# Optimization experiments

Measured on AMD Instinct MI355X. Metric: run time of the kernel, lower is better.

## Reference

```python
import jax, jax.numpy as jnp
import numpy as np

D_MODEL = 192
D_INNER = 384   # expand=2
D_STATE = 16
D_CONV = 4
DT_RANK = 12    # ceil(192/16)
DEPTH = 4
STRIDE = 4
N_PATCH = 400   # 1600 // 4
NCLS = 1000
BATCH = 32
EPS = 1e-5


def setup_inputs() -> dict:
    key = jax.random.key(0)
    ks = iter(jax.random.split(key, 64))
    nrm = lambda shp, s=0.02: jax.random.normal(next(ks), shp, jnp.float32) * s
    inp = {}
    inp["imgs"] = jax.random.normal(next(ks), (BATCH, 1, 40, 40), jnp.float32)
    # StrideEmbed: conv1d(kernel=stride=4) == per-patch linear on [B,400,4]
    inp["patch_w"] = nrm((STRIDE, D_MODEL))
    inp["patch_b"] = jnp.zeros((D_MODEL,), jnp.float32)
    inp["cls_token"] = nrm((1, 1, D_MODEL))
    inp["pos_embed"] = nrm((1, N_PATCH + 1, D_MODEL))
    # per-block Mamba params, stacked on a leading depth axis
    inp["norm_ws"] = jnp.ones((DEPTH, D_MODEL), jnp.float32)
    inp["in_proj_ws"] = nrm((DEPTH, D_MODEL, 2 * D_INNER))
    inp["conv_ws"] = nrm((DEPTH, D_INNER, D_CONV), 0.2)
    inp["conv_bs"] = jnp.zeros((DEPTH, D_INNER), jnp.float32)
    inp["x_proj_ws"] = nrm((DEPTH, D_INNER, DT_RANK + 2 * D_STATE))
    inp["dt_proj_ws"] = nrm((DEPTH, DT_RANK, D_INNER), 0.1)
    # dt bias ~ inverse-softplus of small positive dt
    inp["dt_proj_bs"] = jnp.log(jnp.expm1(jnp.full((DEPTH, D_INNER), 0.01, jnp.float32)))
    inp["A_logs"] = jnp.log(jnp.broadcast_to(
        jnp.arange(1, D_STATE + 1, dtype=jnp.float32), (DEPTH, D_INNER, D_STATE)))
    inp["Ds"] = jnp.ones((DEPTH, D_INNER), jnp.float32)
    inp["out_proj_ws"] = nrm((DEPTH, D_INNER, D_MODEL))
    inp["norm_f_w"] = jnp.ones((D_MODEL,), jnp.float32)
    inp["head_w"] = nrm((D_MODEL, NCLS))
    inp["head_b"] = jnp.zeros((NCLS,), jnp.float32)
    return inp


def rmsnorm(x, w):
    return x * jax.lax.rsqrt(jnp.mean(x * x, axis=-1, keepdims=True) + EPS) * w


def mamba_mixer(x, in_w, conv_w, conv_b, xp_w, dt_w, dt_b, A_log, Dp, out_w):
    # x: [B, L, D_MODEL]
    B, L, _ = x.shape
    xz = x @ in_w                         # [B, L, 2*d_inner]
    u, z = jnp.split(xz, 2, axis=-1)
    # causal depthwise conv1d (kernel 4), truncated to L, then SiLU
    upad = jnp.pad(u, ((0, 0), (D_CONV - 1, 0), (0, 0)))
    uc = sum(upad[:, k:k + L, :] * conv_w[:, k] for k in range(D_CONV)) + conv_b
    uc = jax.nn.silu(uc)
    # input-dependent dt, B, C
    dbl = uc @ xp_w                       # [B, L, dt_rank + 2*d_state]
    dt = dbl[..., :DT_RANK]
    Bm = dbl[..., DT_RANK:DT_RANK + D_STATE]
    Cm = dbl[..., DT_RANK + D_STATE:]
    delta = jax.nn.softplus(dt @ dt_w + dt_b)           # [B, L, d_inner]
    A = -jnp.exp(A_log)                                  # [d_inner, d_state]
    dA = jnp.exp(delta[..., None] * A)                   # [B, L, d_inner, d_state]
    dBu = (delta * uc)[..., None] * Bm[:, :, None, :]    # [B, L, d_inner, d_state]

    def step(h, t):
        da, dbu, c = t
        h = da * h + dbu                                 # [B, d_inner, d_state]
        y = jnp.einsum('bds,bs->bd', h, c)
        return h, y

    h0 = jnp.zeros((B, D_INNER, D_STATE), x.dtype)
    _, ys = jax.lax.scan(step, h0, (jnp.moveaxis(dA, 1, 0),
                                    jnp.moveaxis(dBu, 1, 0),
                                    jnp.moveaxis(Cm, 1, 0)))
    y = jnp.moveaxis(ys, 0, 1) + uc * Dp                 # [B, L, d_inner]
    return (y * jax.nn.silu(z)) @ out_w


def reference(imgs, patch_w, patch_b, cls_token, pos_embed, norm_ws, in_proj_ws,
              conv_ws, conv_bs, x_proj_ws, dt_proj_ws, dt_proj_bs, A_logs, Ds,
              out_proj_ws, norm_f_w, head_w, head_b):
    B = imgs.shape[0]
    seq = imgs.reshape(B, N_PATCH, STRIDE)               # [B, 400, 4] (in_chans=1)
    x = seq @ patch_w + patch_b + pos_embed[:, :-1, :]   # patch embed + pos (cls pos is last)
    cls = cls_token + pos_embed[:, -1:, :]
    x = jnp.concatenate([x, jnp.broadcast_to(cls, (B, 1, D_MODEL))], axis=1)  # cls appended at end
    residual = None
    for i in range(DEPTH):
        residual = x if residual is None else x + residual  # fused add-norm, prenorm
        h = rmsnorm(residual, norm_ws[i])
        x = mamba_mixer(h, in_proj_ws[i], conv_ws[i], conv_bs[i], x_proj_ws[i],
                        dt_proj_ws[i], dt_proj_bs[i], A_logs[i], Ds[i], out_proj_ws[i])
    x = rmsnorm(x + residual, norm_f_w)                   # final fused add-norm, prenorm=False
    return x[:, -1, :] @ head_w + head_b                  # head on cls (last) token
```

## Files before the change

### kernel.cpp

```cpp
#include <hip/hip_runtime.h>
#include <hip/hip_bf16.h>
#include <hip/hip_fp16.h>

using bf16 = __hip_bfloat16;
typedef short short8 __attribute__((ext_vector_type(8)));
typedef float floatx4 __attribute__((ext_vector_type(4)));

#define LSEQ 401
#define NTOK 12832
#define NTOKP 12928
#define DM 192
#define DI 384
#define NB 32
#define NCH 13
#define CHT 32

#define O_IMGS   0
#define O_PW     51200
#define O_PB     51968
#define O_CLS    52160
#define O_POS    52352
#define O_NORMW  129344
#define O_INW    130112
#define O_CONVW  719936
#define O_CONVB  726080
#define O_XPW    727616
#define O_DTW    795200
#define O_DTB    813632
#define O_ALOG   815168
#define O_DS     839744
#define O_OUTW   841280
#define O_NORMF  1136192
#define O_HEADW  1136384
#define O_HEADB  1328384
#define WTOT     1329408

#define BO_INWT  0
#define BO_XPWT  589824
#define BO_OUTWT 688128
#define BFTOT_F  491520

__constant__ int g_sz[18] = {51200, 768, 192, 192, 76992, 768, 589824, 6144, 1536,
                             67584, 18432, 1536, 24576, 1536, 294912, 192, 192000, 1000};
__constant__ int g_off[18] = {O_IMGS, O_PW, O_PB, O_CLS, O_POS, O_NORMW, O_INW, O_CONVW,
                              O_CONVB, O_XPW, O_DTW, O_DTB, O_ALOG, O_DS, O_OUTW,
                              O_NORMF, O_HEADW, O_HEADB};

struct SrcPtrs { const void* p[18]; };

static __device__ __forceinline__ int probe_flag(const unsigned short* probe) {
    unsigned short u0 = probe[0];
    if (u0 == 0x3F80u) return 0;
    if (u0 == 0x3C00u) return 2;
    return 1;
}
static __device__ __forceinline__ float load_src(int flag, const void* p, long i) {
    if (flag == 0) return __bfloat162float(((const bf16*)p)[i]);
    if (flag == 2) return __half2float(((const __half*)p)[i]);
    return ((const float*)p)[i];
}
static __device__ __forceinline__ unsigned short f2b(float f) {
    bf16 h = __float2bfloat16(f);
    return *reinterpret_cast<unsigned short*>(&h);
}
static __device__ __forceinline__ float b2f_us(unsigned short us) {
    unsigned int ui = (unsigned int)us << 16;
    return __uint_as_float(ui);
}

__global__ void convert_kernel(SrcPtrs sp, const unsigned short* __restrict__ probe,
                               float* __restrict__ dst) {
    int flag = probe_flag(probe);
    int which = blockIdx.y;
    int n = g_sz[which];
    const void* src = sp.p[which];
    float* d = dst + g_off[which];
    for (int i = blockIdx.x * blockDim.x + threadIdx.x; i < n; i += gridDim.x * blockDim.x)
        d[i] = load_src(flag, src, i);
}

__global__ void prep_wt_kernel(SrcPtrs sp, const unsigned short* __restrict__ probe,
                               unsigned short* __restrict__ bfw) {
    int flag = probe_flag(probe);
    int which = blockIdx.y, layer = blockIdx.z;
    int i = blockIdx.x * 256 + threadIdx.x;
    if (which == 0) {
        if (i >= 768 * 192) return;
        int n = i / 192, k = i % 192;
        float v = load_src(flag, sp.p[6], (long)layer * 147456 + (long)k * 768 + n);
        bfw[BO_INWT + (long)layer * 147456 + i] = f2b(v);
    } else if (which == 1) {
        if (i >= 64 * 384) return;
        int n = i / 384, k = i % 384;
        float v = (n < 44) ? load_src(flag, sp.p[9], (long)layer * 16896 + (long)k * 44 + n) : 0.f;
        bfw[BO_XPWT + (long)layer * 24576 + i] = f2b(v);
    } else {
        if (i >= 192 * 384) return;
        int n = i / 384, k = i % 384;
        float v = load_src(flag, sp.p[14], (long)layer * 73728 + (long)k * 192 + n);
        bfw[BO_OUTWT + (long)layer * 73728 + i] = f2b(v);
    }
}

__global__ __launch_bounds__(192) void embed_kernel(const float* __restrict__ W, float* __restrict__ x) {
    const float* imgs = W + O_IMGS;
    const float* pw   = W + O_PW;
    int tok = blockIdx.x;
    int b = tok / LSEQ, t = tok % LSEQ;
    int c = threadIdx.x;
    float v;
    if (t < 400) {
        float s0 = imgs[b * 1600 + t * 4 + 0];
        float s1 = imgs[b * 1600 + t * 4 + 1];
        float s2 = imgs[b * 1600 + t * 4 + 2];
        float s3 = imgs[b * 1600 + t * 4 + 3];
        v = s0 * pw[0 * DM + c] + s1 * pw[1 * DM + c] +
            s2 * pw[2 * DM + c] + s3 * pw[3 * DM + c] +
            W[O_PB + c] + W[O_POS + t * DM + c];
    } else {
        v = W[O_CLS + c] + W[O_POS + 400 * DM + c];
    }
    x[(long)tok * DM + c] = v;
}

__global__ __launch_bounds__(256) void resnorm_kernel(
    const float* __restrict__ x, float* __restrict__ res, unsigned short* __restrict__ hbf,
    const float* __restrict__ w, int first) {
    int wv = threadIdx.x >> 6, lane = threadIdx.x & 63;
    long tok = (long)blockIdx.x * 4 + wv;
    long base = tok * DM + lane * 4;
    float4 v = make_float4(0.f, 0.f, 0.f, 0.f);
    bool real = (tok < NTOK);
    if (real && lane < 48) {
        v = *(const float4*)(x + base);
        if (!first) {
            float4 r = *(const float4*)(res + base);
            v.x += r.x; v.y += r.y; v.z += r.z; v.w += r.w;
        }
        *(float4*)(res + base) = v;
    }
    float ss = v.x * v.x + v.y * v.y + v.z * v.z + v.w * v.w;
#pragma unroll
    for (int o = 1; o < 64; o <<= 1) ss += __shfl_xor(ss, o, 64);
    float inv = rsqrtf(ss * (1.f / DM) + 1e-5f);
    if (lane < 48) {
        if (real) {
            float4 w4 = *(const float4*)(w + lane * 4);
            ushort4 h;
            h.x = f2b(v.x * inv * w4.x); h.y = f2b(v.y * inv * w4.y);
            h.z = f2b(v.z * inv * w4.z); h.w = f2b(v.w * inv * w4.w);
            *(ushort4*)(hbf + base) = h;
        } else if (tok < NTOKP) {
            ushort4 h; h.x = h.y = h.z = h.w = 0;
            *(ushort4*)(hbf + base) = h;
        }
    }
}

template <int OUTBF>
__global__ __launch_bounds__(256) void gemm_mfma(
    const unsigned short* __restrict__ A, const unsigned short* __restrict__ Wt,
    void* __restrict__ C, int K, int N, int NC) {
    __shared__ unsigned short sA[64][72];
    __shared__ unsigned short sW[64][72];
    int tid = threadIdx.x;
    int w = tid >> 6, lane = tid & 63;
    int q = lane >> 4, m = lane & 15;
    long tok0 = (long)blockIdx.x * 64;
    int n0 = blockIdx.y * 64;
    floatx4 acc[4] = {};
    for (int k0 = 0; k0 < K; k0 += 64) {
        int slot = tid;
#pragma unroll
        for (int i = 0; i < 2; ++i, slot += 256) {
            int r = slot >> 3, c8 = (slot & 7) * 8;
            *(short8*)&sA[r][c8] = *(const short8*)(A + (tok0 + r) * K + k0 + c8);
            *(short8*)&sW[r][c8] = *(const short8*)(Wt + (long)(n0 + r) * K + k0 + c8);
        }
        __syncthreads();
#pragma unroll
        for (int q2 = 0; q2 < 64; q2 += 32) {
            short8 bfr = *(const short8*)&sA[w * 16 + m][q2 + q * 8];
#pragma unroll
            for (int nt = 0; nt < 4; ++nt) {
                short8 afr = *(const short8*)&sW[nt * 16 + m][q2 + q * 8];
                acc[nt] = __builtin_amdgcn_mfma_f32_16x16x32_bf16(afr, bfr, acc[nt], 0, 0, 0);
            }
        }
        __syncthreads();
    }
    long tok = tok0 + w * 16 + m;
#pragma unroll
    for (int nt = 0; nt < 4; ++nt) {
        int ch = n0 + nt * 16 + q * 4;
        if (OUTBF) {
            unsigned short* dst = (unsigned short*)C + tok * NC + ch;
            ushort4 h4;
            h4.x = f2b(acc[nt][0]); h4.y = f2b(acc[nt][1]);
            h4.z = f2b(acc[nt][2]); h4.w = f2b(acc[nt][3]);
            *(ushort4*)dst = h4;
        } else {
            float* dst = (float*)C + tok * NC + ch;
            if (ch + 3 < N) {
                *(float4*)dst = make_float4(acc[nt][0], acc[nt][1], acc[nt][2], acc[nt][3]);
            } else {
#pragma unroll
                for (int r = 0; r < 4; ++r)
                    if (ch + r < N) dst[r] = acc[nt][r];
            }
        }
    }
}

__global__ __launch_bounds__(256) void gemm_mfma128(
    const unsigned short* __restrict__ A, const unsigned short* __restrict__ Wt,
    unsigned short* __restrict__ C, int K, int NC) {
    __shared__ unsigned short sA[128][72];
    __shared__ unsigned short sW[64][72];
    int tid = threadIdx.x;
    int w = tid >> 6, lane = tid & 63;
    int q = lane >> 4, m = lane & 15;
    long tok0 = (long)blockIdx.x * 128;
    int n0 = blockIdx.y * 64;
    floatx4 acc[2][4] = {};
    for (int k0 = 0; k0 < K; k0 += 64) {
#pragma unroll
        for (int p = 0; p < 4; ++p) {
            int idx = tid + p * 256;
            int r = idx >> 3, c8 = (idx & 7) * 8;
            *(short8*)&sA[r][c8] = *(const short8*)(A + (tok0 + r) * K + k0 + c8);
        }
#pragma unroll
        for (int p = 0; p < 2; ++p) {
            int idx = tid + p * 256;
            int r = idx >> 3, c8 = (idx & 7) * 8;
            *(short8*)&sW[r][c8] = *(const short8*)(Wt + (long)(n0 + r) * K + k0 + c8);
        }
        __syncthreads();
#pragma unroll
        for (int q2 = 0; q2 < 64; q2 += 32) {
#pragma unroll
            for (int tf = 0; tf < 2; ++tf) {
                short8 bfr = *(const short8*)&sA[w * 32 + tf * 16 + m][q2 + q * 8];
#pragma unroll
                for (int nt = 0; nt < 4; ++nt) {
                    short8 afr = *(const short8*)&sW[nt * 16 + m][q2 + q * 8];
                    acc[tf][nt] = __builtin_amdgcn_mfma_f32_16x16x32_bf16(afr, bfr, acc[tf][nt], 0, 0, 0);
                }
            }
        }
        __syncthreads();
    }
#pragma unroll
    for (int tf = 0; tf < 2; ++tf) {
        long tok = tok0 + w * 32 + tf * 16 + m;
#pragma unroll
        for (int nt = 0; nt < 4; ++nt) {
            int ch = n0 + nt * 16 + q * 4;
            ushort4 h4;
            h4.x = f2b(acc[tf][nt][0]); h4.y = f2b(acc[tf][nt][1]);
            h4.z = f2b(acc[tf][nt][2]); h4.w = f2b(acc[tf][nt][3]);
            *(ushort4*)((unsigned short*)C + tok * NC + ch) = h4;
        }
    }
}

__global__ __launch_bounds__(256) void gemm_xproj_conv(
    const unsigned short* __restrict__ xzb, const unsigned short* __restrict__ Wt,
    const float* __restrict__ cw, const float* __restrict__ cb,
    unsigned short* __restrict__ ucb, float* __restrict__ dblP) {
    __shared__ unsigned short sA[64][72];
    __shared__ unsigned short sW[64][72];
    __shared__ float scw[128][4];
    __shared__ float scb[128];
    int tid = threadIdx.x;
    int w = tid >> 6, lane = tid & 63;
    int q = lane >> 4, m = lane & 15;
    long tok0 = (long)blockIdx.x * 64;
    int koff = blockIdx.y * 128;
    float* C = dblP + (long)blockIdx.y * NTOKP * 44;
    if (tid < 128) {
        scb[tid] = cb[koff + tid];
        *(float4*)&scw[tid][0] = *(const float4*)(cw + (koff + tid) * 4);
    }
    floatx4 acc[4] = {};
    for (int k0 = 0; k0 < 128; k0 += 64) {
        if (k0 == 0) __syncthreads();
        int slot = tid;
#pragma unroll
        for (int i = 0; i < 2; ++i, slot += 256) {
            int r = slot >> 3, c8 = (slot & 7) * 8;
            long tok = tok0 + r;
            int t = (int)(tok % LSEQ);
            int lk = k0 + c8;
            int kk = koff + lk;
            float res[8];
#pragma unroll
            for (int jj = 0; jj < 8; ++jj) res[jj] = scb[lk + jj];
#pragma unroll
            for (int j = 0; j < 4; ++j) {
                int off = 3 - j;
                if (t >= off) {
                    short8 v = *(const short8*)(xzb + (tok - off) * 768 + kk);
#pragma unroll
                    for (int jj = 0; jj < 8; ++jj)
                        res[jj] = fmaf(scw[lk + jj][j], b2f_us((unsigned short)v[jj]), res[jj]);
                }
            }
            short8 h8;
#pragma unroll
            for (int jj = 0; jj < 8; ++jj) {
                float sv = res[jj] / (1.f + __expf(-res[jj]));
                h8[jj] = (short)f2b(sv);
            }
            *(short8*)&sA[r][c8] = h8;
            *(short8*)(ucb + tok * DI + kk) = h8;
            *(short8*)&sW[r][c8] = *(const short8*)(Wt + (long)r * DI + koff + k0 + c8);
        }
        __syncthreads();
#pragma unroll
        for (int q2 = 0; q2 < 64; q2 += 32) {
            short8 bfr = *(const short8*)&sA[w * 16 + m][q2 + q * 8];
#pragma unroll
            for (int nt = 0; nt < 4; ++nt) {
                short8 afr = *(const short8*)&sW[nt * 16 + m][q2 + q * 8];
                acc[nt] = __builtin_amdgcn_mfma_f32_16x16x32_bf16(afr, bfr, acc[nt], 0, 0, 0);
            }
        }
        __syncthreads();
    }
    long tok = tok0 + w * 16 + m;
#pragma unroll
    for (int nt = 0; nt < 4; ++nt) {
        int ch = nt * 16 + q * 4;
        float* dst = C + tok * 44 + ch;
        if (ch + 3 < 44) {
            *(float4*)dst = make_float4(acc[nt][0], acc[nt][1], acc[nt][2], acc[nt][3]);
        } else {
#pragma unroll
            for (int r = 0; r < 4; ++r)
                if (ch + r < 44) dst[r] = acc[nt][r];
        }
    }
}

__global__ __launch_bounds__(256) void dbl_sum_kernel(const float* __restrict__ dblP,
                                                      float* __restrict__ dbl) {
    int i = blockIdx.x * 256 + threadIdx.x;
    if (i < NTOK * 44)
        dbl[i] = dblP[i] + dblP[(long)NTOKP * 44 + i] + dblP[(long)2 * NTOKP * 44 + i];
}

__global__ __launch_bounds__(256) void scan_sum_kernel(
    const float* __restrict__ dbl, const unsigned short* __restrict__ ucb,
    const float* __restrict__ dtw, const float* __restrict__ dtb,
    const float* __restrict__ Alog, unsigned short* __restrict__ deltaBuf,
    float* __restrict__ Aprod, float* __restrict__ Hend) {
    int ch = blockIdx.x, b = blockIdx.y;
    int tid = threadIdx.x;
    int shalf = tid & 1;
    int d = blockIdx.z * 128 + (tid >> 1);
    int t0 = ch * CHT;
    long tokb = (long)b * LSEQ + t0;
    int tmax = min(CHT, LSEQ - t0);
    bool last = (ch == NCH - 1);
    __shared__ float sdt[CHT][12];
    __shared__ float sB[CHT][16];
    for (int i = tid; i < tmax * 12; i += 256) {
        int r = i / 12, k = i % 12;
        sdt[r][k] = dbl[(tokb + r) * 44 + k];
    }
    if (!last) {
        for (int i = tid; i < CHT * 16; i += 256) {
            int r = i >> 4, s = i & 15;
            sB[r][s] = dbl[(tokb + r) * 44 + 12 + s];
        }
    }
    float dtwr[12];
#pragma unroll
    for (int k = 0; k < 12; ++k) dtwr[k] = dtw[k * DI + d];
    float bias = dtb[d];
    float a[8];
#pragma unroll
    for (int s = 0; s < 8; ++s) a[s] = -__expf(Alog[d * 16 + shalf * 8 + s]);
    float h[8] = {};
    float sumd = 0.f;
    __syncthreads();
    float u0 = b2f_us(ucb[tokb * DI + d]);
    float u1 = b2f_us(ucb[(tokb + min(1, tmax - 1)) * DI + d]);
#pragma unroll 2
    for (int t = 0; t < tmax; ++t) {
        int tp = min(t + 2, tmax - 1);
        float u2 = b2f_us(ucb[(tokb + tp) * DI + d]);
        float acc = bias;
#pragma unroll
        for (int k = 0; k < 12; ++k) acc = fmaf(sdt[t][k], dtwr[k], acc);
        float delta = (acc > 20.f) ? acc : __logf(1.f + __expf(acc));
        delta = b2f_us(f2b(delta));
        if (shalf == 0) deltaBuf[(tokb + t) * DI + d] = f2b(delta);
        if (!last) {
            float du = delta * u0;
            sumd += delta;
            float Bv[8];
            *(float4*)&Bv[0] = *(const float4*)&sB[t][shalf * 8];
            *(float4*)&Bv[4] = *(const float4*)&sB[t][shalf * 8 + 4];
#pragma unroll
            for (int s = 0; s < 8; ++s) {
                float da = __expf(delta * a[s]);
                h[s] = fmaf(da, h[s], du * Bv[s]);
            }
        }
        u0 = u1; u1 = u2;
    }
    if (!last) {
        long idx = (((long)b * NCH + ch) * DI + d) * 16 + shalf * 8;
        float ap[8], he[8];
#pragma unroll
        for (int s = 0; s < 8; ++s) { ap[s] = __expf(a[s] * sumd); he[s] = h[s]; }
        *(float4*)(Aprod + idx) = *(float4*)&ap[0];
        *(float4*)(Aprod + idx + 4) = *(float4*)&ap[4];
        *(float4*)(Hend + idx) = *(float4*)&he[0];
        *(float4*)(Hend + idx + 4) = *(float4*)&he[4];
    }
}

__global__ __launch_bounds__(256) void scan_combine_kernel(
    const float* __restrict__ Ap, const float* __restrict__ He, float* __restrict__ hinit) {
    long gid = (long)blockIdx.x * 256 + threadIdx.x;
    int b = (int)(gid / 6144);
    int r = (int)(gid % 6144);
    float carry = 0.f;
#pragma unroll
    for (int j = 0; j < NCH; ++j) {
        long idx = ((long)b * NCH + j) * 6144 + r;
        hinit[idx] = carry;
        if (j < NCH - 1) carry = fmaf(Ap[idx], carry, He[idx]);
    }
}

__global__ __launch_bounds__(256) void scan_main_kernel(
    const unsigned short* __restrict__ deltaBuf, const unsigned short* __restrict__ ucb,
    const unsigned short* __restrict__ xzb, const float* __restrict__ Alog,
    const float* __restrict__ Dvec, const float* __restrict__ hinit,
    const float* __restrict__ dbl, unsigned short* __restrict__ ybf) {
    int ch = blockIdx.x, b = blockIdx.y;
    int tid = threadIdx.x;
    int shalf = tid & 1;
    int d = blockIdx.z * 128 + (tid >> 1);
    int t0 = ch * CHT;
    long tokb = (long)b * LSEQ + t0;
    int tmax = min(CHT, LSEQ - t0);
    __shared__ float sB[CHT][16], sC[CHT][16];
    for (int i = tid; i < CHT * 16; i += 256) {
        int r = i >> 4, s = i & 15;
        bool ok = (r < tmax);
        sB[r][s] = ok ? dbl[(tokb + r) * 44 + 12 + s] : 0.f;
        sC[r][s] = ok ? dbl[(tokb + r) * 44 + 28 + s] : 0.f;
    }
    float a[8];
#pragma unroll
    for (int s = 0; s < 8; ++s) a[s] = -__expf(Alog[d * 16 + shalf * 8 + s]);
    float h[8];
    long hidx = (((long)b * NCH + ch) * DI + d) * 16 + shalf * 8;
    *(float4*)&h[0] = *(const float4*)(hinit + hidx);
    *(float4*)&h[4] = *(const float4*)(hinit + hidx + 4);
    float Dp = Dvec[d];
    __syncthreads();
    int t1i = min(1, tmax - 1);
    float d0 = b2f_us(deltaBuf[tokb * DI + d]);
    float u0 = b2f_us(ucb[tokb * DI + d]);
    float z0 = b2f_us(xzb[tokb * 768 + DI + d]);
    float d1 = b2f_us(deltaBuf[(tokb + t1i) * DI + d]);
    float u1 = b2f_us(ucb[(tokb + t1i) * DI + d]);
    float z1 = b2f_us(xzb[(tokb + t1i) * 768 + DI + d]);
#pragma unroll 2
    for (int t = 0; t < tmax; ++t) {
        int tp = min(t + 2, tmax - 1);
        float d2 = b2f_us(deltaBuf[(tokb + tp) * DI + d]);
        float u2 = b2f_us(ucb[(tokb + tp) * DI + d]);
        float z2 = b2f_us(xzb[(tokb + tp) * 768 + DI + d]);
        float Bv[8], Cv[8];
        *(float4*)&Bv[0] = *(const float4*)&sB[t][shalf * 8];
        *(float4*)&Bv[4] = *(const float4*)&sB[t][shalf * 8 + 4];
        *(float4*)&Cv[0] = *(const float4*)&sC[t][shalf * 8];
        *(float4*)&Cv[4] = *(const float4*)&sC[t][shalf * 8 + 4];
        float du = d0 * u0;
        float y0 = 0.f, y1 = 0.f, y2 = 0.f, y3 = 0.f;
#pragma unroll
        for (int s = 0; s < 8; s += 4) {
            float da0 = __expf(d0 * a[s]);
            float da1 = __expf(d0 * a[s + 1]);
            float da2 = __expf(d0 * a[s + 2]);
            float da3 = __expf(d0 * a[s + 3]);
            h[s]     = fmaf(da0, h[s],     du * Bv[s]);
            h[s + 1] = fmaf(da1, h[s + 1], du * Bv[s + 1]);
            h[s + 2] = fmaf(da2, h[s + 2], du * Bv[s + 2]);
            h[s + 3] = fmaf(da3, h[s + 3], du * Bv[s + 3]);
            y0 = fmaf(h[s],     Cv[s],     y0);
            y1 = fmaf(h[s + 1], Cv[s + 1], y1);
            y2 = fmaf(h[s + 2], Cv[s + 2], y2);
            y3 = fmaf(h[s + 3], Cv[s + 3], y3);
        }
        float p = (y0 + y1) + (y2 + y3);
        p += __shfl_xor(p, 1, 64);
        if (shalf == 0) {
            float y = fmaf(u0, Dp, p);
            float gz = z0 / (1.f + __expf(-z0));
            ybf[(tokb + t) * DI + d] = f2b(y * gz);
        }
        d0 = d1; u0 = u1; z0 = z1;
        d1 = d2; u1 = u2; z1 = z2;
    }
}

__global__ __launch_bounds__(256) void finalnorm_kernel(
    const float* __restrict__ x, const float* __restrict__ res,
    const float* __restrict__ w, float* __restrict__ v) {
    int b = blockIdx.x;
    int c = threadIdx.x;
    long tok = (long)b * LSEQ + 400;
    __shared__ float sb[256];
    float val = 0.f;
    if (c < DM) val = x[tok * DM + c] + res[tok * DM + c];
    sb[c] = val * val;
    __syncthreads();
    for (int o = 128; o > 0; o >>= 1) {
        if (c < o) sb[c] += sb[c + o];
        __syncthreads();
    }
    float inv = rsqrtf(sb[0] * (1.f / DM) + 1e-5f);
    if (c < DM) v[b * DM + c] = val * inv * w[c];
}

__global__ __launch_bounds__(128) void head_kernel(
    const float* __restrict__ v, const float* __restrict__ hw, const float* __restrict__ hb,
    const unsigned short* __restrict__ probe, void* __restrict__ out) {
    int b = blockIdx.y;
    int n = blockIdx.x * 128 + threadIdx.x;
    __shared__ float vs[DM];
    for (int i = threadIdx.x; i < DM; i += 128) vs[i] = v[b * DM + i];
    __syncthreads();
    if (n < 1000) {
        float acc = hb[n];
#pragma unroll 4
        for (int c = 0; c < DM; ++c) acc = fmaf(vs[c], hw[c * 1000 + n], acc);
        int flag = probe_flag(probe);
        if (flag == 0)      ((bf16*)out)[b * 1000 + n] = (bf16)acc;
        else if (flag == 2) ((__half*)out)[b * 1000 + n] = __float2half(acc);
        else                ((float*)out)[b * 1000 + n] = acc;
    }
}

extern "C" void kernel_launch(void* const* d_in, const int* in_sizes, int n_in,
                              void* d_out, int out_size, void* d_ws, size_t ws_size,
                              hipStream_t stream) {
    float* ws = (float*)d_ws;
    float* Wr = ws;
    unsigned short* bfw = (unsigned short*)(ws + WTOT);
    float* act   = ws + WTOT + BFTOT_F;
    float* resT  = act;
    float* xB    = resT + (long)NTOKP * DM;
    float* dbl   = xB + (long)NTOKP * DM;
    float* dblP  = dbl + (long)NTOKP * 44;
    float* Aprod = dblP + (long)3 * NTOKP * 44;
    float* Hend  = Aprod + (long)NB * NCH * 6144;
    float* hinit = Hend + (long)NB * NCH * 6144;
    float* vbuf  = hinit + (long)NB * NCH * 6144;
    unsigned short* deltaB = (unsigned short*)(vbuf + NB * DM);
    unsigned short* hbf = deltaB + (long)NTOKP * DI;
    unsigned short* xzb = hbf + (long)NTOKP * DM;
    unsigned short* ucb = xzb + (long)NTOKP * 768;
    unsigned short* ybf = ucb + (long)NTOKP * DI;

    const unsigned short* probe = (const unsigned short*)d_in[5];

    SrcPtrs sp;
    for (int i = 0; i < 18; ++i) sp.p[i] = d_in[i];
    convert_kernel<<<dim3(64, 18), 256, 0, stream>>>(sp, probe, Wr);
    prep_wt_kernel<<<dim3(576, 3, 4), 256, 0, stream>>>(sp, probe, bfw);

    embed_kernel<<<NTOK, 192, 0, stream>>>(Wr, xB);

    for (int i = 0; i < 4; ++i) {
        resnorm_kernel<<<NTOKP / 4, 256, 0, stream>>>(xB, resT, hbf, Wr + O_NORMW + i * DM, i == 0);
        gemm_mfma128<<<dim3(101, 12), 256, 0, stream>>>(
            hbf, bfw + BO_INWT + (long)i * 147456, xzb, 192, 768);
        gemm_xproj_conv<<<dim3(202, 3), 256, 0, stream>>>(
            xzb, bfw + BO_XPWT + (long)i * 24576,
            Wr + O_CONVW + i * 1536, Wr + O_CONVB + i * DI, ucb, dblP);
        dbl_sum_kernel<<<(NTOK * 44 + 255) / 256, 256, 0, stream>>>(dblP, dbl);
        scan_sum_kernel<<<dim3(NCH, NB, 3), 256, 0, stream>>>(
            dbl, ucb, Wr + O_DTW + i * 4608, Wr + O_DTB + i * DI,
            Wr + O_ALOG + i * 6144, deltaB, Aprod, Hend);
        scan_combine_kernel<<<(NB * 6144) / 256, 256, 0, stream>>>(Aprod, Hend, hinit);
        scan_main_kernel<<<dim3(NCH, NB, 3), 256, 0, stream>>>(
            deltaB, ucb, xzb, Wr + O_ALOG + i * 6144, Wr + O_DS + i * DI,
            hinit, dbl, ybf);
        gemm_mfma<0><<<dim3(202, 3), 256, 0, stream>>>(
            ybf, bfw + BO_OUTWT + (long)i * 73728, xB, 384, 192, 192);
    }

    finalnorm_kernel<<<NB, 256, 0, stream>>>(xB, resT, Wr + O_NORMF, vbuf);
    head_kernel<<<dim3(8, NB), 128, 0, stream>>>(vbuf, Wr + O_HEADW, Wr + O_HEADB, probe, d_out);
}
```

Before: 624.4 us.

## Fold split-K reduction, scan combine and final norm into consumer kernels

Removes the dbl_sum kernel by having the scan kernels sum the three split-K partial slabs directly when loading dt/B/C into shared memory. Removes the scan_combine kernel by having each scan_main block serially fold the preceding chunks' Aprod/Hend into its own initial state. Fuses the final RMSNorm into the head kernel. This cuts three launches per layer plus intermediate buffer traffic, at the cost of redundant reads (3x partial loads in two kernels, up to 12 chunk folds per block).

```diff
diff --git a/kernel.cpp b/kernel.cpp
--- a/kernel.cpp
+++ b/kernel.cpp
@@ -14,6 +14,7 @@
 #define NB 32
 #define NCH 13
 #define CHT 32
+#define SLAB ((long)NTOKP * 44)
 
 #define O_IMGS   0
 #define O_PW     51200
@@ -344,15 +345,8 @@
     }
 }
 
-__global__ __launch_bounds__(256) void dbl_sum_kernel(const float* __restrict__ dblP,
-                                                      float* __restrict__ dbl) {
-    int i = blockIdx.x * 256 + threadIdx.x;
-    if (i < NTOK * 44)
-        dbl[i] = dblP[i] + dblP[(long)NTOKP * 44 + i] + dblP[(long)2 * NTOKP * 44 + i];
-}
-
 __global__ __launch_bounds__(256) void scan_sum_kernel(
-    const float* __restrict__ dbl, const unsigned short* __restrict__ ucb,
+    const float* __restrict__ dblP, const unsigned short* __restrict__ ucb,
     const float* __restrict__ dtw, const float* __restrict__ dtb,
     const float* __restrict__ Alog, unsigned short* __restrict__ deltaBuf,
     float* __restrict__ Aprod, float* __restrict__ Hend) {
@@ -368,12 +362,14 @@
     __shared__ float sB[CHT][16];
     for (int i = tid; i < tmax * 12; i += 256) {
         int r = i / 12, k = i % 12;
-        sdt[r][k] = dbl[(tokb + r) * 44 + k];
+        long o = (tokb + r) * 44 + k;
+        sdt[r][k] = dblP[o] + dblP[o + SLAB] + dblP[o + 2 * SLAB];
     }
     if (!last) {
         for (int i = tid; i < CHT * 16; i += 256) {
             int r = i >> 4, s = i & 15;
-            sB[r][s] = dbl[(tokb + r) * 44 + 12 + s];
+            long o = (tokb + r) * 44 + 12 + s;
+            sB[r][s] = dblP[o] + dblP[o + SLAB] + dblP[o + 2 * SLAB];
         }
     }
     float dtwr[12];
@@ -424,25 +420,12 @@
     }
 }
 
-__global__ __launch_bounds__(256) void scan_combine_kernel(
-    const float* __restrict__ Ap, const float* __restrict__ He, float* __restrict__ hinit) {
-    long gid = (long)blockIdx.x * 256 + threadIdx.x;
-    int b = (int)(gid / 6144);
-    int r = (int)(gid % 6144);
-    float carry = 0.f;
-#pragma unroll
-    for (int j = 0; j < NCH; ++j) {
-        long idx = ((long)b * NCH + j) * 6144 + r;
-        hinit[idx] = carry;
-        if (j < NCH - 1) carry = fmaf(Ap[idx], carry, He[idx]);
-    }
-}
-
 __global__ __launch_bounds__(256) void scan_main_kernel(
     const unsigned short* __restrict__ deltaBuf, const unsigned short* __restrict__ ucb,
     const unsigned short* __restrict__ xzb, const float* __restrict__ Alog,
-    const float* __restrict__ Dvec, const float* __restrict__ hinit,
-    const float* __restrict__ dbl, unsigned short* __restrict__ ybf) {
+    const float* __restrict__ Dvec, const float* __restrict__ Aprod,
+    const float* __restrict__ Hend, const float* __restrict__ dblP,
+    unsigned short* __restrict__ ybf) {
     int ch = blockIdx.x, b = blockIdx.y;
     int tid = threadIdx.x;
     int shalf = tid & 1;
@@ -453,17 +436,29 @@
     __shared__ float sB[CHT][16], sC[CHT][16];
     for (int i = tid; i < CHT * 16; i += 256) {
         int r = i >> 4, s = i & 15;
-        bool ok = (r < tmax);
-        sB[r][s] = ok ? dbl[(tokb + r) * 44 + 12 + s] : 0.f;
-        sC[r][s] = ok ? dbl[(tokb + r) * 44 + 28 + s] : 0.f;
+        if (r < tmax) {
+            long o = (tokb + r) * 44 + 12 + s;
+            sB[r][s] = dblP[o] + dblP[o + SLAB] + dblP[o + 2 * SLAB];
+            long o2 = o + 16;
+            sC[r][s] = dblP[o2] + dblP[o2 + SLAB] + dblP[o2 + 2 * SLAB];
+        } else {
+            sB[r][s] = 0.f; sC[r][s] = 0.f;
+        }
     }
     float a[8];
 #pragma unroll
     for (int s = 0; s < 8; ++s) a[s] = -__expf(Alog[d * 16 + shalf * 8 + s]);
-    float h[8];
-    long hidx = (((long)b * NCH + ch) * DI + d) * 16 + shalf * 8;
-    *(float4*)&h[0] = *(const float4*)(hinit + hidx);
-    *(float4*)&h[4] = *(const float4*)(hinit + hidx + 4);
+    float h[8] = {};
+    for (int j = 0; j < ch; ++j) {
+        long idx = (((long)b * NCH + j) * DI + d) * 16 + shalf * 8;
+        float ap[8], he[8];
+        *(float4*)&ap[0] = *(const float4*)(Aprod + idx);
+        *(float4*)&ap[4] = *(const float4*)(Aprod + idx + 4);
+        *(float4*)&he[0] = *(const float4*)(Hend + idx);
+        *(float4*)&he[4] = *(const float4*)(Hend + idx + 4);
+#pragma unroll
+        for (int s = 0; s < 8; ++s) h[s] = fmaf(ap[s], h[s], he[s]);
+    }
     float Dp = Dvec[d];
     __syncthreads();
     int t1i = min(1, tmax - 1);
@@ -513,32 +508,28 @@
     }
 }
 
-__global__ __launch_bounds__(256) void finalnorm_kernel(
+__global__ __launch_bounds__(128) void head_kernel(
     const float* __restrict__ x, const float* __restrict__ res,
-    const float* __restrict__ w, float* __restrict__ v) {
-    int b = blockIdx.x;
-    int c = threadIdx.x;
-    long tok = (long)b * LSEQ + 400;
-    __shared__ float sb[256];
-    float val = 0.f;
-    if (c < DM) val = x[tok * DM + c] + res[tok * DM + c];
-    sb[c] = val * val;
-    __syncthreads();
-    for (int o = 128; o > 0; o >>= 1) {
-        if (c < o) sb[c] += sb[c + o];
-        __syncthreads();
-    }
-    float inv = rsqrtf(sb[0] * (1.f / DM) + 1e-5f);
-    if (c < DM) v[b * DM + c] = val * inv * w[c];
-}
-
-__global__ __launch_bounds__(128) void head_kernel(
-    const float* __restrict__ v, const float* __restrict__ hw, const float* __restrict__ hb,
-    const unsigned short* __restrict__ probe, void* __restrict__ out) {
+    const float* __restrict__ nf, const float* __restrict__ hw,
+    const float* __restrict__ hb, const unsigned short* __restrict__ probe,
+    void* __restrict__ out) {
     int b = blockIdx.y;
     int n = blockIdx.x * 128 + threadIdx.x;
+    long tok = (long)b * LSEQ + 400;
     __shared__ float vs[DM];
-    for (int i = threadIdx.x; i < DM; i += 128) vs[i] = v[b * DM + i];
+    __shared__ float red[2];
+    float ss = 0.f;
+    for (int i = threadIdx.x; i < DM; i += 128) {
+        float v = x[tok * DM + i] + res[tok * DM + i];
+        vs[i] = v;
+        ss = fmaf(v, v, ss);
+    }
+#pragma unroll
+    for (int o = 1; o < 64; o <<= 1) ss += __shfl_xor(ss, o, 64);
+    if ((threadIdx.x & 63) == 0) red[threadIdx.x >> 6] = ss;
+    __syncthreads();
+    float inv = rsqrtf((red[0] + red[1]) * (1.f / DM) + 1e-5f);
+    for (int i = threadIdx.x; i < DM; i += 128) vs[i] = vs[i] * inv * nf[i];
     __syncthreads();
     if (n < 1000) {
         float acc = hb[n];
@@ -560,13 +551,10 @@
     float* act   = ws + WTOT + BFTOT_F;
     float* resT  = act;
     float* xB    = resT + (long)NTOKP * DM;
-    float* dbl   = xB + (long)NTOKP * DM;
-    float* dblP  = dbl + (long)NTOKP * 44;
-    float* Aprod = dblP + (long)3 * NTOKP * 44;
+    float* dblP  = xB + (long)NTOKP * DM;
+    float* Aprod = dblP + 3 * SLAB;
     float* Hend  = Aprod + (long)NB * NCH * 6144;
-    float* hinit = Hend + (long)NB * NCH * 6144;
-    float* vbuf  = hinit + (long)NB * NCH * 6144;
-    unsigned short* deltaB = (unsigned short*)(vbuf + NB * DM);
+    unsigned short* deltaB = (unsigned short*)(Hend + (long)NB * NCH * 6144);
     unsigned short* hbf = deltaB + (long)NTOKP * DI;
     unsigned short* xzb = hbf + (long)NTOKP * DM;
     unsigned short* ucb = xzb + (long)NTOKP * 768;
@@ -588,18 +576,16 @@
         gemm_xproj_conv<<<dim3(202, 3), 256, 0, stream>>>(
             xzb, bfw + BO_XPWT + (long)i * 24576,
             Wr + O_CONVW + i * 1536, Wr + O_CONVB + i * DI, ucb, dblP);
-        dbl_sum_kernel<<<(NTOK * 44 + 255) / 256, 256, 0, stream>>>(dblP, dbl);
         scan_sum_kernel<<<dim3(NCH, NB, 3), 256, 0, stream>>>(
-            dbl, ucb, Wr + O_DTW + i * 4608, Wr + O_DTB + i * DI,
+            dblP, ucb, Wr + O_DTW + i * 4608, Wr + O_DTB + i * DI,
             Wr + O_ALOG + i * 6144, deltaB, Aprod, Hend);
-        scan_combine_kernel<<<(NB * 6144) / 256, 256, 0, stream>>>(Aprod, Hend, hinit);
         scan_main_kernel<<<dim3(NCH, NB, 3), 256, 0, stream>>>(
             deltaB, ucb, xzb, Wr + O_ALOG + i * 6144, Wr + O_DS + i * DI,
-            hinit, dbl, ybf);
+            Aprod, Hend, dblP, ybf);
         gemm_mfma<0><<<dim3(202, 3), 256, 0, stream>>>(
             ybf, bfw + BO_OUTWT + (long)i * 73728, xB, 384, 192, 192);
     }
 
-    finalnorm_kernel<<<NB, 256, 0, stream>>>(xB, resT, Wr + O_NORMF, vbuf);
-    head_kernel<<<dim3(8, NB), 128, 0, stream>>>(vbuf, Wr + O_HEADW, Wr + O_HEADB, probe, d_out);
-}
+    head_kernel<<<dim3(8, NB), 128, 0, stream>>>(
+        xB, resT, Wr + O_NORMF, Wr + O_HEADW, Wr + O_HEADB, probe, d_out);
+}
```

Result: slower. 637.9 us (+2.2%).
